# Kernel optimization log

Measured on AMD Instinct MI355X. Metric: run time of the kernel, lower is better.

The kernel has to match this reference:

```python
import jax, jax.numpy as jnp
import numpy as np

B, S, D, H, FF = 2, 2048, 1024, 16, 4096
DK = D // H
MAX_SEQ_LEN = 2048
THETA = 10000.0
EPS = 1e-5


def _linear_init(key, out_f, in_f):
    std = (2.0 / (in_f + out_f)) ** 0.5
    return std * jax.random.truncated_normal(key, -3.0, 3.0, (out_f, in_f), dtype=jnp.float32)


def setup_inputs() -> dict:
    key = jax.random.key(0)
    ks = jax.random.split(key, 9)
    x = jax.random.normal(ks[0], (B, S, D), dtype=jnp.float32)
    token_positions = jnp.broadcast_to(jnp.arange(S, dtype=jnp.int32)[None, :], (B, S))
    return {
        "x": x,
        "wq": _linear_init(ks[1], D, D),
        "wk": _linear_init(ks[2], D, D),
        "wv": _linear_init(ks[3], D, D),
        "wo": _linear_init(ks[4], D, D),
        "w1": _linear_init(ks[5], FF, D),
        "w2": _linear_init(ks[6], D, FF),
        "w3": _linear_init(ks[7], FF, D),
        "g1": jnp.ones((D,), dtype=jnp.float32),
        "g2": jnp.ones((D,), dtype=jnp.float32),
        "token_positions": token_positions,
    }


def _rmsnorm(x, g):
    x32 = x.astype(jnp.float32)
    ms = jnp.sqrt(jnp.mean(x32 * x32, axis=-1, keepdims=True) + EPS)
    return ((x32 / ms) * g).astype(x.dtype)


def _rope(x, pos):
    # x: (B, H, S, DK); pos: (B, S)
    inv_freq = 1.0 / THETA ** (jnp.arange(0, DK, 2, dtype=jnp.float32) / DK)  # (DK/2,)
    freqs = pos.astype(jnp.float32)[..., None] * inv_freq  # (B, S, DK/2)
    cos = jnp.cos(freqs)[:, None, :, :]  # (B, 1, S, DK/2) broadcast over heads
    sin = jnp.sin(freqs)[:, None, :, :]
    x_real = x[..., 0::2]
    x_imag = x[..., 1::2]
    rot_real = x_real * cos - x_imag * sin
    rot_imag = x_real * sin + x_imag * cos
    return jnp.stack([rot_real, rot_imag], axis=-1).reshape(x.shape)


def reference(x, wq, wk, wv, wo, w1, w2, w3, g1, g2, token_positions):
    # --- attention sublayer ---
    h = _rmsnorm(x, g1)
    def proj(w):
        y = jnp.einsum('bsd,ed->bse', h, w)
        return y.reshape(B, S, H, DK).transpose(0, 2, 1, 3)  # (B,H,S,DK)
    Q = _rope(proj(wq), token_positions)
    K = _rope(proj(wk), token_positions)
    V = proj(wv)
    scores = jnp.einsum('bhqd,bhkd->bhqk', Q, K)  # (B,H,S,S) full matrix (naive)
    causal = jnp.tril(jnp.ones((S, S), dtype=bool))
    scores = jnp.where(causal, scores, -jnp.inf) / (DK ** 0.5)
    probs = jax.nn.softmax(scores, axis=-1)
    attn = jnp.einsum('bhqk,bhkd->bhqd', probs, V)
    attn = attn.transpose(0, 2, 1, 3).reshape(B, S, D)
    attn = jnp.einsum('bsd,ed->bse', attn, wo)
    y = x + attn
    # --- SwiGLU FFN sublayer ---
    h2 = _rmsnorm(y, g2)
    a = jnp.einsum('bsd,fd->bsf', h2, w1)
    gate = jnp.einsum('bsd,fd->bsf', h2, w3)
    ff = jnp.einsum('bsf,df->bsd', a * jax.nn.sigmoid(a) * gate, w2)
    return y + ff
```

## Files before the change

kernel.cpp:

```cpp
#include <hip/hip_runtime.h>
#include <hip/hip_bf16.h>

#define B_ 2
#define S_ 2048
#define D_ 1024
#define H_ 16
#define DK_ 64
#define FF_ 4096
#define M_ (B_ * S_)

typedef unsigned short u16;
typedef __bf16 bf16x8 __attribute__((ext_vector_type(8)));
typedef float f32x4 __attribute__((ext_vector_type(4)));
typedef u16 u16x4 __attribute__((ext_vector_type(4)));
typedef u16 u16x8 __attribute__((ext_vector_type(8)));

__device__ __forceinline__ u16 f2bf(float f) {
  __bf16 b = (__bf16)f;
  return __builtin_bit_cast(u16, b);
}
__device__ __forceinline__ float bf2f(u16 u) {
  __bf16 b = __builtin_bit_cast(__bf16, u);
  return (float)b;
}

__device__ __forceinline__ void async_lds16(const void* g, void* l) {
  __builtin_amdgcn_global_load_lds(
      (const __attribute__((address_space(1))) unsigned int*)g,
      (__attribute__((address_space(3))) unsigned int*)l, 16, 0, 0);
}

__device__ __forceinline__ void raw_barrier() {
  asm volatile("s_barrier" ::: "memory");
}
#define VMCNT_WAIT(n) asm volatile("s_waitcnt vmcnt(" #n ")" ::: "memory")

__global__ __launch_bounds__(256) void f2b_all(
    const float* __restrict__ wq, const float* __restrict__ wk,
    const float* __restrict__ wv, const float* __restrict__ wo,
    const float* __restrict__ w1, const float* __restrict__ w2,
    const float* __restrict__ w3, u16* __restrict__ wqkvb,
    u16* __restrict__ wob, u16* __restrict__ w1b, u16* __restrict__ w2b,
    u16* __restrict__ w3b) {
  int i4 = blockIdx.x * 256 + threadIdx.x;
  const float* src;
  u16* dst;
  int off;
  if (i4 < 262144) { src = wq; dst = wqkvb; off = i4; }
  else if (i4 < 524288) { src = wk; dst = wqkvb + 1048576; off = i4 - 262144; }
  else if (i4 < 786432) { src = wv; dst = wqkvb + 2097152; off = i4 - 524288; }
  else if (i4 < 1048576) { src = wo; dst = wob; off = i4 - 786432; }
  else if (i4 < 2097152) { src = w1; dst = w1b; off = i4 - 1048576; }
  else if (i4 < 3145728) { src = w2; dst = w2b; off = i4 - 2097152; }
  else { src = w3; dst = w3b; off = i4 - 3145728; }
  float4 v = ((const float4*)src)[off];
  u16x4 o;
  o[0] = f2bf(v.x); o[1] = f2bf(v.y); o[2] = f2bf(v.z); o[3] = f2bf(v.w);
  *(u16x4*)(dst + (size_t)off * 4) = o;
}

__global__ __launch_bounds__(256) void rmsnorm_k(const float* __restrict__ X,
                                                 const float* __restrict__ G,
                                                 u16* __restrict__ Out) {
  const int row = blockIdx.x, tid = threadIdx.x;
  const float4 xv = *(const float4*)(X + (size_t)row * D_ + tid * 4);
  float ss = xv.x * xv.x + xv.y * xv.y + xv.z * xv.z + xv.w * xv.w;
#pragma unroll
  for (int off = 1; off < 64; off <<= 1) ss += __shfl_xor(ss, off);
  __shared__ float red[4];
  if ((tid & 63) == 0) red[tid >> 6] = ss;
  __syncthreads();
  const float tot = red[0] + red[1] + red[2] + red[3];
  const float sc = rsqrtf(tot * (1.0f / D_) + 1e-5f);
  const float4 gv = *(const float4*)(G + tid * 4);
  u16x4 o;
  o[0] = f2bf(xv.x * sc * gv.x);
  o[1] = f2bf(xv.y * sc * gv.y);
  o[2] = f2bf(xv.z * sc * gv.z);
  o[3] = f2bf(xv.w * sc * gv.w);
  *(u16x4*)(Out + (size_t)row * D_ + tid * 4) = o;
}

__global__ __launch_bounds__(256) void rope2_k(unsigned int* __restrict__ Qb,
                                               unsigned int* __restrict__ Kb,
                                               const int* __restrict__ pos) {
  int idx = blockIdx.x * 256 + threadIdx.x;
  unsigned int* buf = Qb;
  float scale = 0.125f;
  if (idx >= 2097152) { buf = Kb; scale = 1.f; idx -= 2097152; }
  const int row = idx >> 9, p = idx & 511;
  const int i = p & 31;
  unsigned int v = buf[(size_t)row * 512 + p];
  const float xr = bf2f((u16)(v & 0xffffu));
  const float xi = bf2f((u16)(v >> 16));
  const float ang =
      (float)pos[row] * __expf(-(float)i * (9.210340371976184f / 32.0f));
  float sn, cs;
  sincosf(ang, &sn, &cs);
  const float orr = (xr * cs - xi * sn) * scale;
  const float oii = (xr * sn + xi * cs) * scale;
  buf[(size_t)row * 512 + p] =
      (unsigned int)f2bf(orr) | ((unsigned int)f2bf(oii) << 16);
}

__global__ __launch_bounds__(256) void transpose_v(const u16* __restrict__ V,
                                                   u16* __restrict__ Vt) {
  __shared__ __align__(16) u16 tile[32][64];
  const int tid = threadIdx.x;
  const int s0 = blockIdx.x * 32, bh = blockIdx.y, b = bh >> 4, h = bh & 15;
  {
    const int sr = tid >> 3, c = tid & 7;
    *(u16x8*)&tile[sr][c * 8] =
        *(const u16x8*)(V + (size_t)(b * S_ + s0 + sr) * D_ + h * DK_ + c * 8);
  }
  __syncthreads();
  {
    const int dk = tid >> 2, cs = tid & 3;
    u16x8 vv;
#pragma unroll
    for (int j = 0; j < 8; ++j) vv[j] = tile[cs * 8 + j][dk];
    *(u16x8*)(Vt + (size_t)(bh * DK_ + dk) * S_ + s0 + cs * 8) = vv;
  }
}

template <int BM, int BN, int BK, int EPI>
__global__ __launch_bounds__(512) void gemm2ph(const u16* __restrict__ A,
                                               const u16* __restrict__ Bw,
                                               void* __restrict__ Cout,
                                               const void* __restrict__ auxp,
                                               int N, int K) {
  constexpr int CPR = BK / 8;
  constexpr int ACH = BM * CPR;
  constexpr int TCH = (BM + BN) * CPR;
  constexpr int MR = BM / 32, NR = BN / 64;
  static_assert(TCH / 512 == 8, "vmcnt(8) assumes 8 loads/thread per STAGE");
  __shared__ __align__(16) u16 As[2][BM * BK];
  __shared__ __align__(16) u16 Bs[2][BN * BK];
  const int tid = threadIdx.x, l = tid & 63, w = tid >> 6;
  const int gx = gridDim.x;
  const int nwg = gx * (int)gridDim.y;
  const int id = blockIdx.y * gx + blockIdx.x;
  const int swz = (id & 7) * (nwg >> 3) + (id >> 3);
  const int m0 = (swz / gx) * BM, n0 = (swz % gx) * BN;
  const int wm = (w >> 2) * (BM / 2), wn = (w & 3) * (BN / 4);
  const int lr = l & 15, lg = l >> 4;

  f32x4 acc[MR][NR] = {};

  auto STAGE = [&](int bf, int k0) {
#pragma unroll
    for (int i = 0; i < TCH / 512; ++i) {
      const int s = i * 512 + tid;
      const int base = i * 512 + w * 64;
      if (base < ACH) {
        const int r = s / CPR, ch = s % CPR;
        async_lds16(A + (size_t)(m0 + r) * K + k0 + ((ch ^ (r & 7)) * 8),
                    (char*)As[bf] + base * 16);
      } else {
        const int s2 = s - ACH;
        const int r = s2 / CPR, ch = s2 % CPR;
        async_lds16(Bw + (size_t)(n0 + r) * K + k0 + ((ch ^ (r & 7)) * 8),
                    (char*)Bs[bf] + (base - ACH) * 16);
      }
    }
  };

  STAGE(0, 0);
  int cur = 0;
  for (int k0 = 0; k0 < K; k0 += BK) {
    if (k0 + BK < K) {
      STAGE(cur ^ 1, k0 + BK);
      VMCNT_WAIT(8);
    } else {
      VMCNT_WAIT(0);
    }
    raw_barrier();
#pragma unroll
    for (int kk = 0; kk < BK / 32; ++kk) {
      bf16x8 af[MR], bfr[NR];
#pragma unroll
      for (int i = 0; i < MR; ++i) {
        const int row = wm + i * 16 + lr;
        af[i] = *(const bf16x8*)&As[cur][row * BK +
                                         (((kk * 4 + lg) ^ (row & 7)) * 8)];
      }
#pragma unroll
      for (int j = 0; j < NR; ++j) {
        const int row = wn + j * 16 + lr;
        bfr[j] = *(const bf16x8*)&Bs[cur][row * BK +
                                          (((kk * 4 + lg) ^ (row & 7)) * 8)];
      }
      __builtin_amdgcn_s_setprio(1);
#pragma unroll
      for (int i = 0; i < MR; ++i)
#pragma unroll
        for (int j = 0; j < NR; ++j)
          acc[i][j] = __builtin_amdgcn_mfma_f32_16x16x32_bf16(
              af[i], bfr[j], acc[i][j], 0, 0, 0);
      __builtin_amdgcn_s_setprio(0);
    }
    raw_barrier();
    cur ^= 1;
  }

#pragma unroll
  for (int i = 0; i < MR; ++i) {
#pragma unroll
    for (int j = 0; j < NR; ++j) {
#pragma unroll
      for (int t = 0; t < 4; ++t) {
        const int grow = m0 + wm + i * 16 + lg * 4 + t;
        const int gcol = n0 + wn + j * 16 + lr;
        const float v = acc[i][j][t];
        if (EPI == 0) {
          ((u16*)Cout)[(size_t)grow * N + gcol] = f2bf(v);
        } else if (EPI == 1) {
          const size_t idx = (size_t)grow * N + gcol;
          ((float*)Cout)[idx] = ((const float*)auxp)[idx] + v;
        } else if (EPI == 2) {
          const size_t idx = (size_t)grow * N + gcol;
          const float av = bf2f(((const u16*)auxp)[idx]);
          const float sw = av / (1.f + __expf(-av));
          ((u16*)Cout)[idx] = f2bf(sw * v);
        } else {
          u16* base = (u16*)Cout + (size_t)(gcol >> 10) * ((size_t)M_ * D_);
          base[(size_t)grow * D_ + (gcol & 1023)] = f2bf(v);
        }
      }
    }
  }
}

__global__ __launch_bounds__(256) void attn_fwd(const u16* __restrict__ Q,
                                                const u16* __restrict__ K,
                                                const u16* __restrict__ Vt,
                                                u16* __restrict__ O) {
  __shared__ __align__(16) u16 Ks[2][64 * 64];
  __shared__ __align__(16) u16 Vs[2][64 * 64];
  __shared__ __align__(16) u16 Ps[4][16 * 72];
  const int tid = threadIdx.x, l = tid & 63, w = tid >> 6;
  const int lr = l & 15, lg = l >> 4;
  const int bid = blockIdx.x;
  const int xcd = bid & 7, i = bid >> 3;
  const int bh = xcd * 4 + (i >> 5);
  const int qx = 31 - (i & 31);
  const int b = bh >> 4, h = bh & 15;
  const int q0w = qx * 64 + w * 16;

  const u16* Kb = K + (size_t)(b * S_) * D_ + h * DK_;
  const u16* Vb = Vt + (size_t)bh * DK_ * S_;

  bf16x8 aq[2];
  {
    const u16* qp = Q + (size_t)(b * S_ + q0w + lr) * D_ + h * DK_ + lg * 8;
    aq[0] = *(const bf16x8*)qp;
    aq[1] = *(const bf16x8*)(qp + 32);
  }
  f32x4 oacc[4] = {};
  float mrow[4], lrow[4];
#pragma unroll
  for (int t = 0; t < 4; ++t) { mrow[t] = -1e30f; lrow[t] = 0.f; }

  u16x8 ones_u;
#pragma unroll
  for (int j = 0; j < 8; ++j) ones_u[j] = 0x3F80;
  const bf16x8 ones = __builtin_bit_cast(bf16x8, ones_u);

  const int ntiles = qx + 1;

  auto STAGE = [&](int bf, int t) {
#pragma unroll
    for (int inst = 0; inst < 2; ++inst) {
      const int s = (w * 2 + inst) * 64 + l;
      const int r = s >> 3, ch = s & 7;
      const int chs = ch ^ (r & 7);
      async_lds16(Kb + (size_t)(t * 64 + r) * D_ + chs * 8,
                  (char*)Ks[bf] + (w * 2 + inst) * 1024);
      async_lds16(Vb + (size_t)r * S_ + t * 64 + chs * 8,
                  (char*)Vs[bf] + (w * 2 + inst) * 1024);
    }
  };

  STAGE(0, 0);
  __syncthreads();
  int cur = 0;
  for (int it = 0; it < ntiles; ++it) {
    if (it + 1 < ntiles) STAGE(cur ^ 1, it + 1);
    f32x4 sf[4];
    __builtin_amdgcn_s_setprio(1);
#pragma unroll
    for (int n = 0; n < 4; ++n) {
      const int kvr = n * 16 + lr;
      f32x4 z = {};
      bf16x8 bk0 = *(const bf16x8*)&Ks[cur][kvr * 64 + ((lg ^ (kvr & 7)) * 8)];
      bf16x8 bk1 =
          *(const bf16x8*)&Ks[cur][kvr * 64 + (((4 + lg) ^ (kvr & 7)) * 8)];
      z = __builtin_amdgcn_mfma_f32_16x16x32_bf16(aq[0], bk0, z, 0, 0, 0);
      z = __builtin_amdgcn_mfma_f32_16x16x32_bf16(aq[1], bk1, z, 0, 0, 0);
      sf[n] = z;
    }
    __builtin_amdgcn_s_setprio(0);
    if (it < qx) {
      float fm[4];
      bool exc = false;
#pragma unroll
      for (int t = 0; t < 4; ++t) {
        fm[t] = fmaxf(fmaxf(sf[0][t], sf[1][t]), fmaxf(sf[2][t], sf[3][t]));
        exc |= fm[t] > mrow[t] + 8.f;
      }
      if (__any(exc)) {
#pragma unroll
        for (int t = 0; t < 4; ++t) {
          float mx = fm[t];
#pragma unroll
          for (int off = 1; off < 16; off <<= 1)
            mx = fmaxf(mx, __shfl_xor(mx, off));
          const float nm = fmaxf(mrow[t], mx);
          const float c = __expf(mrow[t] - nm);
          mrow[t] = nm;
          lrow[t] *= c;
#pragma unroll
          for (int d = 0; d < 4; ++d) oacc[d][t] *= c;
        }
      }
#pragma unroll
      for (int t = 0; t < 4; ++t)
#pragma unroll
        for (int n = 0; n < 4; ++n)
          Ps[w][(lg * 4 + t) * 72 + n * 16 + lr] =
              f2bf(__expf(sf[n][t] - mrow[t]));
    } else {
      const int kv0 = it * 64;
#pragma unroll
      for (int t = 0; t < 4; ++t) {
        const int qrow = q0w + lg * 4 + t;
        float v[4];
#pragma unroll
        for (int n = 0; n < 4; ++n)
          v[n] = (kv0 + n * 16 + lr <= qrow) ? sf[n][t] : -1e30f;
        float mx = fmaxf(fmaxf(v[0], v[1]), fmaxf(v[2], v[3]));
#pragma unroll
        for (int off = 1; off < 16; off <<= 1)
          mx = fmaxf(mx, __shfl_xor(mx, off));
        const float nm = fmaxf(mrow[t], mx);
        const float c = __expf(mrow[t] - nm);
        mrow[t] = nm;
        lrow[t] *= c;
#pragma unroll
        for (int d = 0; d < 4; ++d) oacc[d][t] *= c;
#pragma unroll
        for (int n = 0; n < 4; ++n)
          Ps[w][(lg * 4 + t) * 72 + n * 16 + lr] = f2bf(__expf(v[n] - nm));
      }
    }
    bf16x8 ap0 = *(const bf16x8*)&Ps[w][lr * 72 + lg * 8];
    bf16x8 ap1 = *(const bf16x8*)&Ps[w][lr * 72 + 32 + lg * 8];
    __builtin_amdgcn_s_setprio(1);
    f32x4 zs = {};
    zs = __builtin_amdgcn_mfma_f32_16x16x32_bf16(ap0, ones, zs, 0, 0, 0);
    zs = __builtin_amdgcn_mfma_f32_16x16x32_bf16(ap1, ones, zs, 0, 0, 0);
#pragma unroll
    for (int d = 0; d < 4; ++d) {
      const int row = d * 16 + lr;
      bf16x8 bv0 = *(const bf16x8*)&Vs[cur][row * 64 + ((lg ^ (row & 7)) * 8)];
      bf16x8 bv1 =
          *(const bf16x8*)&Vs[cur][row * 64 + (((4 + lg) ^ (row & 7)) * 8)];
      oacc[d] = __builtin_amdgcn_mfma_f32_16x16x32_bf16(ap0, bv0, oacc[d], 0, 0, 0);
      oacc[d] = __builtin_amdgcn_mfma_f32_16x16x32_bf16(ap1, bv1, oacc[d], 0, 0, 0);
    }
    __builtin_amdgcn_s_setprio(0);
#pragma unroll
    for (int t = 0; t < 4; ++t) lrow[t] += zs[t];
    __syncthreads();
    cur ^= 1;
  }
#pragma unroll
  for (int d = 0; d < 4; ++d) {
#pragma unroll
    for (int t = 0; t < 4; ++t) {
      const size_t idx =
          (size_t)(b * S_ + q0w + lg * 4 + t) * D_ + h * DK_ + d * 16 + lr;
      O[idx] = f2bf(oacc[d][t] / lrow[t]);
    }
  }
}

extern "C" void kernel_launch(void* const* d_in, const int* in_sizes, int n_in,
                              void* d_out, int out_size, void* d_ws,
                              size_t ws_size, hipStream_t stream) {
  (void)in_sizes; (void)n_in; (void)out_size; (void)ws_size;
  const float* x = (const float*)d_in[0];
  const float* wq = (const float*)d_in[1];
  const float* wk = (const float*)d_in[2];
  const float* wv = (const float*)d_in[3];
  const float* wo = (const float*)d_in[4];
  const float* w1 = (const float*)d_in[5];
  const float* w2 = (const float*)d_in[6];
  const float* w3 = (const float*)d_in[7];
  const float* g1 = (const float*)d_in[8];
  const float* g2 = (const float*)d_in[9];
  const int* tp = (const int*)d_in[10];
  float* out = (float*)d_out;

  char* ws = (char*)d_ws;
  const size_t MB = 1024u * 1024u;
  u16* wqkvb = (u16*)(ws + 0 * MB);
  u16* wob = (u16*)(ws + 6 * MB);
  u16* w1b = (u16*)(ws + 8 * MB);
  u16* w2b = (u16*)(ws + 16 * MB);
  u16* w3b = (u16*)(ws + 24 * MB);
  u16* hb  = (u16*)(ws + 32 * MB);
  float* yb = (float*)(ws + 40 * MB);
  u16* h2b = (u16*)(ws + 56 * MB);
  u16* Qb  = (u16*)(ws + 64 * MB);
  u16* Kb  = (u16*)(ws + 72 * MB);
  u16* Vb  = (u16*)(ws + 80 * MB);
  u16* Vtb = (u16*)(ws + 88 * MB);
  u16* ab  = (u16*)(ws + 64 * MB);
  u16* ffb = (u16*)(ws + 96 * MB);
  u16* aob = hb;

  f2b_all<<<16384, 256, 0, stream>>>(wq, wk, wv, wo, w1, w2, w3, wqkvb, wob,
                                     w1b, w2b, w3b);

  rmsnorm_k<<<4096, 256, 0, stream>>>(x, g1, hb);

  gemm2ph<256, 256, 64, 3><<<dim3(12, 16), 512, 0, stream>>>(
      hb, wqkvb, Qb, nullptr, 3072, 1024);

  rope2_k<<<16384, 256, 0, stream>>>((unsigned int*)Qb, (unsigned int*)Kb, tp);
  transpose_v<<<dim3(64, 32), 256, 0, stream>>>(Vb, Vtb);

  attn_fwd<<<1024, 256, 0, stream>>>(Qb, Kb, Vtb, aob);

  gemm2ph<128, 128, 128, 1><<<dim3(8, 32), 512, 0, stream>>>(aob, wob, yb, x,
                                                             1024, 1024);
  rmsnorm_k<<<4096, 256, 0, stream>>>(yb, g2, h2b);

  gemm2ph<256, 256, 64, 0><<<dim3(16, 16), 512, 0, stream>>>(
      h2b, w1b, ab, nullptr, 4096, 1024);
  gemm2ph<256, 256, 64, 2><<<dim3(16, 16), 512, 0, stream>>>(h2b, w3b, ffb, ab,
                                                             4096, 1024);
  gemm2ph<128, 128, 128, 1><<<dim3(8, 32), 512, 0, stream>>>(ffb, w2b, out, yb,
                                                             1024, 4096);
}
```

Baseline: 292.6 us.

## Add 256x256 GEMM kernel with loads interleaved across four MFMA phases

Adds a specialised 256x256x64 GEMM kernel that splits each K-step into four phases. The next tile's global-to-LDS loads are spread across the first three phases and issued between the LDS fragment reads and the MFMA blocks, with wave priority raised during the MFMAs. It replaces the previous two-phase kernel for the QKV projection and the two FFN up-projections, aiming to overlap memory traffic with matrix math better. The cost is extra barriers per K-step and a full vmcnt wait at the end of each step.

Measured after the change: 284.9 us. -2.6%, faster.

```diff
diff --git a/kernel.cpp b/kernel.cpp
--- a/kernel.cpp
+++ b/kernel.cpp
@@ -123,6 +123,118 @@
   }
 }
 
+template <int EPI>
+__global__ __launch_bounds__(512) void gemm8ph(const u16* __restrict__ A,
+                                               const u16* __restrict__ Bw,
+                                               void* __restrict__ Cout,
+                                               const void* __restrict__ auxp,
+                                               int N, int K) {
+  constexpr int BM = 256, BN = 256, BK = 64;
+  constexpr int CPR = BK / 8;
+  constexpr int ACH = BM * CPR;
+  __shared__ __align__(16) u16 As[2][BM * BK];
+  __shared__ __align__(16) u16 Bs[2][BN * BK];
+  const int tid = threadIdx.x, l = tid & 63, w = tid >> 6;
+  const int gx = gridDim.x;
+  const int nwg = gx * (int)gridDim.y;
+  const int id = blockIdx.y * gx + blockIdx.x;
+  const int swz = (id & 7) * (nwg >> 3) + (id >> 3);
+  const int m0 = (swz / gx) * BM, n0 = (swz % gx) * BN;
+  const int wm = (w >> 2) * 128, wn = (w & 3) * 64;
+  const int lr = l & 15, lg = l >> 4;
+
+  f32x4 acc[8][4] = {};
+
+  auto STAGE_PART = [&](int bf, int k0, int i0, int i1) {
+    for (int i = i0; i < i1; ++i) {
+      const int s = i * 512 + tid;
+      const int base = i * 512 + w * 64;
+      if (base < ACH) {
+        const int r = s / CPR, ch = s % CPR;
+        async_lds16(A + (size_t)(m0 + r) * K + k0 + ((ch ^ (r & 7)) * 8),
+                    (char*)As[bf] + base * 16);
+      } else {
+        const int s2 = s - ACH;
+        const int r = s2 / CPR, ch = s2 % CPR;
+        async_lds16(Bw + (size_t)(n0 + r) * K + k0 + ((ch ^ (r & 7)) * 8),
+                    (char*)Bs[bf] + (base - ACH) * 16);
+      }
+    }
+  };
+
+  STAGE_PART(0, 0, 0, 8);
+  VMCNT_WAIT(0);
+  raw_barrier();
+  int cur = 0;
+  for (int k0 = 0; k0 < K; k0 += BK) {
+    const bool more = (k0 + BK) < K;
+    bf16x8 bfr[4];
+#pragma unroll
+    for (int ph = 0; ph < 4; ++ph) {
+      const int kk = ph >> 1, iq = ph & 1;
+      if (iq == 0) {
+#pragma unroll
+        for (int j = 0; j < 4; ++j) {
+          const int row = wn + j * 16 + lr;
+          bfr[j] = *(const bf16x8*)&Bs[cur][row * BK +
+                                            (((kk * 4 + lg) ^ (row & 7)) * 8)];
+        }
+      }
+      bf16x8 af[4];
+#pragma unroll
+      for (int i = 0; i < 4; ++i) {
+        const int row = wm + (iq * 4 + i) * 16 + lr;
+        af[i] = *(const bf16x8*)&As[cur][row * BK +
+                                         (((kk * 4 + lg) ^ (row & 7)) * 8)];
+      }
+      if (more) {
+        if (ph == 0) STAGE_PART(cur ^ 1, k0 + BK, 0, 3);
+        else if (ph == 1) STAGE_PART(cur ^ 1, k0 + BK, 3, 6);
+        else if (ph == 2) STAGE_PART(cur ^ 1, k0 + BK, 6, 8);
+      }
+      raw_barrier();
+      __builtin_amdgcn_s_setprio(1);
+#pragma unroll
+      for (int i = 0; i < 4; ++i)
+#pragma unroll
+        for (int j = 0; j < 4; ++j)
+          acc[iq * 4 + i][j] = __builtin_amdgcn_mfma_f32_16x16x32_bf16(
+              af[i], bfr[j], acc[iq * 4 + i][j], 0, 0, 0);
+      __builtin_amdgcn_s_setprio(0);
+      if (ph < 3) raw_barrier();
+    }
+    if (more) {
+      VMCNT_WAIT(0);
+      raw_barrier();
+    }
+    cur ^= 1;
+  }
+
+#pragma unroll
+  for (int i = 0; i < 8; ++i) {
+#pragma unroll
+    for (int j = 0; j < 4; ++j) {
+#pragma unroll
+      for (int t = 0; t < 4; ++t) {
+        const int grow = m0 + wm + i * 16 + lg * 4 + t;
+        const int gcol = n0 + wn + j * 16 + lr;
+        const float v = acc[i][j][t];
+        if (EPI == 0) {
+          ((u16*)Cout)[(size_t)grow * N + gcol] = f2bf(v);
+        } else if (EPI == 2) {
+          const size_t idx = (size_t)grow * N + gcol;
+          const float av = bf2f(((const u16*)auxp)[idx]);
+          const float sw = av / (1.f + __expf(-av));
+          ((u16*)Cout)[idx] = f2bf(sw * v);
+        } else {
+          u16* base = (u16*)Cout + (size_t)(gcol >> 10) * ((size_t)M_ * D_);
+          base[(size_t)grow * D_ + (gcol & 1023)] = f2bf(v);
+        }
+      }
+    }
+  }
+}
+
 template <int BM, int BN, int BK, int EPI>
 __global__ __launch_bounds__(512) void gemm2ph(const u16* __restrict__ A,
                                                const u16* __restrict__ Bw,
@@ -217,14 +329,6 @@
         } else if (EPI == 1) {
           const size_t idx = (size_t)grow * N + gcol;
           ((float*)Cout)[idx] = ((const float*)auxp)[idx] + v;
-        } else if (EPI == 2) {
-          const size_t idx = (size_t)grow * N + gcol;
-          const float av = bf2f(((const u16*)auxp)[idx]);
-          const float sw = av / (1.f + __expf(-av));
-          ((u16*)Cout)[idx] = f2bf(sw * v);
-        } else {
-          u16* base = (u16*)Cout + (size_t)(gcol >> 10) * ((size_t)M_ * D_);
-          base[(size_t)grow * D_ + (gcol & 1023)] = f2bf(v);
         }
       }
     }
@@ -425,8 +529,8 @@
 
   rmsnorm_k<<<4096, 256, 0, stream>>>(x, g1, hb);
 
-  gemm2ph<256, 256, 64, 3><<<dim3(12, 16), 512, 0, stream>>>(
-      hb, wqkvb, Qb, nullptr, 3072, 1024);
+  gemm8ph<3><<<dim3(12, 16), 512, 0, stream>>>(hb, wqkvb, Qb, nullptr, 3072,
+                                               1024);
 
   rope2_k<<<16384, 256, 0, stream>>>((unsigned int*)Qb, (unsigned int*)Kb, tp);
   transpose_v<<<dim3(64, 32), 256, 0, stream>>>(Vb, Vtb);
@@ -437,10 +541,9 @@
                                                              1024, 1024);
   rmsnorm_k<<<4096, 256, 0, stream>>>(yb, g2, h2b);
 
-  gemm2ph<256, 256, 64, 0><<<dim3(16, 16), 512, 0, stream>>>(
-      h2b, w1b, ab, nullptr, 4096, 1024);
-  gemm2ph<256, 256, 64, 2><<<dim3(16, 16), 512, 0, stream>>>(h2b, w3b, ffb, ab,
-                                                             4096, 1024);
+  gemm8ph<0><<<dim3(16, 16), 512, 0, stream>>>(h2b, w1b, ab, nullptr, 4096,
+                                               1024);
+  gemm8ph<2><<<dim3(16, 16), 512, 0, stream>>>(h2b, w3b, ffb, ab, 4096, 1024);
   gemm2ph<128, 128, 128, 1><<<dim3(8, 32), 512, 0, stream>>>(ffb, w2b, out, yb,
                                                              1024, 4096);
 }
```
